# Performance work log

Measured on AMD Instinct MI355X. Metric: run time of the kernel, lower is better.

## Reference

```python
import jax, jax.numpy as jnp
import numpy as np
from jax import lax

EMB = 1024      # emb_size
H = 2 * EMB     # step_feature_width / LSTM units
B = 1024        # batch of paths
PATH_LEN = 11   # max_path_length=5 -> 5 LSTM steps
N_ENT = 100000


def setup_inputs() -> dict:
    key = jax.random.key(0)
    ks = jax.random.split(key, 8)
    s = lambda fan_in: 1.0 / np.sqrt(fan_in)
    return {
        "path": jax.random.randint(ks[0], (B, PATH_LEN), 0, N_ENT, dtype=jnp.int32),
        "emb_table": jax.random.normal(ks[1], (N_ENT, EMB), jnp.float32),
        "W_lstm": jax.random.normal(ks[2], (2 * EMB, 4 * H), jnp.float32) * s(2 * EMB),
        "U_lstm": jax.random.normal(ks[3], (H, 4 * H), jnp.float32) * s(H),
        "b_lstm": jnp.zeros((4 * H,), jnp.float32),
        "W1": jax.random.normal(ks[4], (H, 2 * EMB), jnp.float32) * s(H),
        "b1": jnp.zeros((2 * EMB,), jnp.float32),
        "W2": jax.random.normal(ks[5], (2 * EMB, 2 * EMB), jnp.float32) * s(2 * EMB),
        "b2": jnp.zeros((2 * EMB,), jnp.float32),
        "W3": jax.random.normal(ks[6], (2 * EMB, 2), jnp.float32) * s(2 * EMB),
        "b3": jnp.zeros((2,), jnp.float32),
    }


def reference(path, emb_table, W_lstm, U_lstm, b_lstm, W1, b1, W2, b2, W3, b3):
    # Gather all entity embeddings along each path: [B, PATH_LEN, EMB]
    vecs = emb_table[path]
    # Step t (t=1..5, i=2t) uses concat(vec(path[i-1]), vec(path[i])): [T, B, 2*EMB]
    x_prev = vecs[:, 1:-1:2, :]   # path[1], path[3], ...  -> [B, T, EMB]
    x_curr = vecs[:, 2::2, :]     # path[2], path[4], ...  -> [B, T, EMB]
    xs = jnp.swapaxes(jnp.concatenate([x_prev, x_curr], axis=-1), 0, 1)  # [T, B, 2E]

    def step(carry, x):
        h, c = carry
        z = x @ W_lstm + h @ U_lstm + b_lstm           # [B, 4H]
        i, f, g, o = jnp.split(z, 4, axis=-1)           # Keras gate order i,f,g,o
        i = jax.nn.sigmoid(i)
        f = jax.nn.sigmoid(f)
        g = jnp.tanh(g)
        o = jax.nn.sigmoid(o)
        c = f * c + i * g
        h = o * jnp.tanh(c)
        return (h, c), None

    h0 = jnp.zeros((xs.shape[1], H), xs.dtype)
    (h, _), _ = lax.scan(step, (h0, h0), xs)

    # 2-layer ReLU MLP + softmax head
    a = jax.nn.relu(h @ W1 + b1)
    a = jax.nn.relu(a @ W2 + b2)
    probs = jax.nn.softmax(a @ W3 + b3, axis=-1)        # [B, 2]
    return probs
```

## Files before the change

### kernel.cpp

```cpp
#include <hip/hip_runtime.h>
#include <hip/hip_bf16.h>

typedef unsigned short u16;
typedef short bf16x8 __attribute__((ext_vector_type(8)));
typedef float floatx4 __attribute__((ext_vector_type(4)));
typedef unsigned short u16x4 __attribute__((ext_vector_type(4)));
typedef unsigned short u16x8 __attribute__((ext_vector_type(8)));

__device__ __forceinline__ u16 f2bf(float f) {
    unsigned int x; __builtin_memcpy(&x, &f, 4);
    unsigned int r = x + 0x7fffu + ((x >> 16) & 1u);
    return (u16)(r >> 16);
}
__device__ __forceinline__ float sigm(float x) {
    return 1.f / (1.f + __expf(-x));
}
__device__ __forceinline__ float tanhx(float x) {
    x = fminf(fmaxf(x, -15.f), 15.f);
    float e = __expf(2.f * x);
    return (e - 1.f) / (e + 1.f);
}

__device__ __forceinline__ int permc(int c) {
    int gate = c >> 11, j = c & 2047;
    return ((j >> 4) << 6) | (gate << 4) | (j & 15);
}

__device__ __forceinline__ void async16(const void* g, void* l) {
    __builtin_amdgcn_global_load_lds(
        (__attribute__((address_space(1))) void*)(void*)(g),
        (__attribute__((address_space(3))) void*)(l),
        16, 0, 0);
}

template <bool PERM>
__global__ __launch_bounds__(256) void transpose_f32_bf16(
    const float* __restrict__ in, u16* __restrict__ out, int K, int N)
{
    __shared__ float tile[64][65];
    const int n0 = blockIdx.x * 64, k0 = blockIdx.y * 64;
    const int t = threadIdx.x;
    const int tc = t & 15, tr = t >> 4;
#pragma unroll
    for (int i = 0; i < 4; i++) {
        int k = i * 16 + tr;
        int n = tc * 4;
        float4 v = *(const float4*)&in[(size_t)(k0 + k) * N + n0 + n];
        tile[k][n + 0] = v.x; tile[k][n + 1] = v.y;
        tile[k][n + 2] = v.z; tile[k][n + 3] = v.w;
    }
    __syncthreads();
#pragma unroll
    for (int i = 0; i < 4; i++) {
        int n = i * 16 + tr;
        int k = tc * 4;
        u16x4 v;
        v.x = f2bf(tile[k + 0][n]);
        v.y = f2bf(tile[k + 1][n]);
        v.z = f2bf(tile[k + 2][n]);
        v.w = f2bf(tile[k + 3][n]);
        const int row = PERM ? permc(n0 + n) : (n0 + n);
        *(u16x4*)&out[(size_t)row * K + k0 + k] = v;
    }
}

__global__ __launch_bounds__(256) void gather_x(
    const int* __restrict__ path, const float* __restrict__ emb, u16* __restrict__ X)
{
    const int blk = blockIdx.x;
    const int t = blk >> 10, b = blk & 1023;
    const int tt = threadIdx.x;
    const int half = tt >> 7;
    const int idx = path[b * 11 + 1 + 2 * t + half];
    const int j = (tt & 127) * 8;
    const float4 v0 = *(const float4*)&emb[(size_t)idx * 1024 + j];
    const float4 v1 = *(const float4*)&emb[(size_t)idx * 1024 + j + 4];
    u16x8 o;
    o[0] = f2bf(v0.x); o[1] = f2bf(v0.y); o[2] = f2bf(v0.z); o[3] = f2bf(v0.w);
    o[4] = f2bf(v1.x); o[5] = f2bf(v1.y); o[6] = f2bf(v1.z); o[7] = f2bf(v1.w);
    *(u16x8*)&X[(size_t)blk * 2048 + half * 1024 + j] = o;
}

__global__ __launch_bounds__(256, 2) void gemm_zx(
    const u16* __restrict__ A, const u16* __restrict__ Bt,
    const float* __restrict__ bias, float* __restrict__ Cf, int M, int N, int K)
{
    __shared__ alignas(16) u16 sA[128 * 32];
    __shared__ alignas(16) u16 sB[128 * 32];
    const int t = threadIdx.x;
    const int lane = t & 63;
    const int w = t >> 6;
    const int wr = w >> 1, wc = w & 1;
    const int l15 = lane & 15, quad = lane >> 4;
    const int m0 = blockIdx.x * 128, n0 = blockIdx.y * 128;
    const int ch1 = t, ch2 = t + 256;
    const int r1 = ch1 >> 2, c1 = (ch1 & 3) * 8;
    const int r2 = ch2 >> 2, c2 = (ch2 & 3) * 8;

    floatx4 acc[4][4] = {};
    for (int k0 = 0; k0 < K; k0 += 32) {
        async16(A + (size_t)(m0 + r1) * K + k0 + c1, sA + ch1 * 8);
        async16(A + (size_t)(m0 + r2) * K + k0 + c2, sA + ch2 * 8);
        async16(Bt + (size_t)(n0 + r1) * K + k0 + c1, sB + ch1 * 8);
        async16(Bt + (size_t)(n0 + r2) * K + k0 + c2, sB + ch2 * 8);
        __syncthreads();
        bf16x8 af[4], bfr[4];
#pragma unroll
        for (int mi = 0; mi < 4; mi++)
            af[mi] = *(const bf16x8*)&sA[(wr * 64 + mi * 16 + l15) * 32 + quad * 8];
#pragma unroll
        for (int ni = 0; ni < 4; ni++)
            bfr[ni] = *(const bf16x8*)&sB[(wc * 64 + ni * 16 + l15) * 32 + quad * 8];
#pragma unroll
        for (int mi = 0; mi < 4; mi++)
#pragma unroll
            for (int ni = 0; ni < 4; ni++)
                acc[mi][ni] = __builtin_amdgcn_mfma_f32_16x16x32_bf16(
                    af[mi], bfr[ni], acc[mi][ni], 0, 0, 0);
        __syncthreads();
    }
#pragma unroll
    for (int mi = 0; mi < 4; mi++) {
#pragma unroll
        for (int ni = 0; ni < 4; ni++) {
            const int n = n0 + wc * 64 + ni * 16 + l15;
            const float bv = bias[(((n >> 4) & 3) << 11) | ((n >> 6) << 4) | (n & 15)];
#pragma unroll
            for (int r = 0; r < 4; r++) {
                const int m = m0 + wr * 64 + mi * 16 + quad * 4 + r;
                Cf[(size_t)m * N + n] = acc[mi][ni][r] + bv;
            }
        }
    }
}

__global__ __launch_bounds__(256, 2) void gemm_step(
    const u16* __restrict__ hin, const u16* __restrict__ Bt,
    const float* __restrict__ Zx, float* __restrict__ c, u16* __restrict__ hout)
{
    const int M = 1024, N = 8192, K = 2048;
    __shared__ alignas(16) u16 sA[128 * 32];
    __shared__ alignas(16) u16 sB[128 * 32];
    const int t = threadIdx.x;
    const int lane = t & 63;
    const int w = t >> 6;
    const int wr = w >> 1, wc = w & 1;
    const int l15 = lane & 15, quad = lane >> 4;
    const int m0 = blockIdx.x * 128, n0 = blockIdx.y * 128;
    const int ch1 = t, ch2 = t + 256;
    const int r1 = ch1 >> 2, c1 = (ch1 & 3) * 8;
    const int r2 = ch2 >> 2, c2 = (ch2 & 3) * 8;

    floatx4 acc[4][4] = {};
    for (int k0 = 0; k0 < K; k0 += 32) {
        async16(hin + (size_t)(m0 + r1) * K + k0 + c1, sA + ch1 * 8);
        async16(hin + (size_t)(m0 + r2) * K + k0 + c2, sA + ch2 * 8);
        async16(Bt + (size_t)(n0 + r1) * K + k0 + c1, sB + ch1 * 8);
        async16(Bt + (size_t)(n0 + r2) * K + k0 + c2, sB + ch2 * 8);
        __syncthreads();
        bf16x8 af[4], bfr[4];
#pragma unroll
        for (int mi = 0; mi < 4; mi++)
            af[mi] = *(const bf16x8*)&sA[(wr * 64 + mi * 16 + l15) * 32 + quad * 8];
#pragma unroll
        for (int ni = 0; ni < 4; ni++)
            bfr[ni] = *(const bf16x8*)&sB[(wc * 64 + ni * 16 + l15) * 32 + quad * 8];
#pragma unroll
        for (int mi = 0; mi < 4; mi++)
#pragma unroll
            for (int ni = 0; ni < 4; ni++)
                acc[mi][ni] = __builtin_amdgcn_mfma_f32_16x16x32_bf16(
                    af[mi], bfr[ni], acc[mi][ni], 0, 0, 0);
        __syncthreads();
    }

    const int jg = (n0 >> 6) + wc;
    const int j = jg * 16 + l15;
#pragma unroll
    for (int mi = 0; mi < 4; mi++) {
#pragma unroll
        for (int r = 0; r < 4; r++) {
            const int m = m0 + wr * 64 + mi * 16 + quad * 4 + r;
            const size_t zb = (size_t)m * N + jg * 64 + l15;
            const float zi = acc[mi][0][r] + Zx[zb];
            const float zf = acc[mi][1][r] + Zx[zb + 16];
            const float zg = acc[mi][2][r] + Zx[zb + 32];
            const float zo = acc[mi][3][r] + Zx[zb + 48];
            const float i_ = sigm(zi);
            const float f_ = sigm(zf);
            const float g_ = tanhx(zg);
            const float o_ = sigm(zo);
            const size_t cb = (size_t)m * 2048 + j;
            const float cn = f_ * c[cb] + i_ * g_;
            c[cb] = cn;
            hout[cb] = f2bf(o_ * tanhx(cn));
        }
    }
}

__global__ __launch_bounds__(256) void gate0(
    const float* __restrict__ Zx, float* __restrict__ c, u16* __restrict__ h)
{
    const int idx = blockIdx.x * 256 + threadIdx.x;
    const int b = idx >> 9;
    const int j = (idx & 511) * 4;
    const size_t base = (size_t)b * 8192 + ((j >> 4) << 6) + (j & 15);
    const float4 vi = *(const float4*)&Zx[base];
    const float4 vf = *(const float4*)&Zx[base + 16];
    const float4 vg = *(const float4*)&Zx[base + 32];
    const float4 vo = *(const float4*)&Zx[base + 48];
    float ia[4] = {vi.x, vi.y, vi.z, vi.w};
    float fa[4] = {vf.x, vf.y, vf.z, vf.w};
    float ga[4] = {vg.x, vg.y, vg.z, vg.w};
    float oa[4] = {vo.x, vo.y, vo.z, vo.w};
    float cn[4]; u16x4 hv;
#pragma unroll
    for (int q = 0; q < 4; q++) {
        (void)fa;
        const float i_ = sigm(ia[q]);
        const float g_ = tanhx(ga[q]);
        const float o_ = sigm(oa[q]);
        cn[q] = i_ * g_;
        hv[q] = f2bf(o_ * tanhx(cn[q]));
        (void)sigm(fa[q]);
    }
    const size_t cb = (size_t)b * 2048 + j;
    *(float4*)&c[cb] = make_float4(cn[0], cn[1], cn[2], cn[3]);
    *(u16x4*)&h[cb] = hv;
}

__global__ __launch_bounds__(256, 4) void gemm_mlp(
    const u16* __restrict__ A, const u16* __restrict__ Bt,
    const float* __restrict__ bias, u16* __restrict__ Cb, int K)
{
    const int N = 2048;
    __shared__ alignas(16) u16 sA[64 * 32];
    __shared__ alignas(16) u16 sB[128 * 32];
    const int t = threadIdx.x;
    const int lane = t & 63;
    const int w = t >> 6;
    const int wr = w >> 1, wc = w & 1;
    const int l15 = lane & 15, quad = lane >> 4;
    const int m0 = blockIdx.x * 64, n0 = blockIdx.y * 128;
    const int rA = t >> 2, cA = (t & 3) * 8;
    const int r1 = t >> 2, c1 = (t & 3) * 8;
    const int r2 = (t + 256) >> 2, c2 = ((t + 256) & 3) * 8;

    floatx4 acc[2][4] = {};
    for (int k0 = 0; k0 < K; k0 += 32) {
        async16(A + (size_t)(m0 + rA) * K + k0 + cA, sA + t * 8);
        async16(Bt + (size_t)(n0 + r1) * K + k0 + c1, sB + t * 8);
        async16(Bt + (size_t)(n0 + r2) * K + k0 + c2, sB + (t + 256) * 8);
        __syncthreads();
        bf16x8 af[2], bfr[4];
#pragma unroll
        for (int mi = 0; mi < 2; mi++)
            af[mi] = *(const bf16x8*)&sA[(wr * 32 + mi * 16 + l15) * 32 + quad * 8];
#pragma unroll
        for (int ni = 0; ni < 4; ni++)
            bfr[ni] = *(const bf16x8*)&sB[(wc * 64 + ni * 16 + l15) * 32 + quad * 8];
#pragma unroll
        for (int mi = 0; mi < 2; mi++)
#pragma unroll
            for (int ni = 0; ni < 4; ni++)
                acc[mi][ni] = __builtin_amdgcn_mfma_f32_16x16x32_bf16(
                    af[mi], bfr[ni], acc[mi][ni], 0, 0, 0);
        __syncthreads();
    }
#pragma unroll
    for (int mi = 0; mi < 2; mi++) {
#pragma unroll
        for (int ni = 0; ni < 4; ni++) {
            const int n = n0 + wc * 64 + ni * 16 + l15;
            const float bv = bias[n];
#pragma unroll
            for (int r = 0; r < 4; r++) {
                const int m = m0 + wr * 32 + mi * 16 + quad * 4 + r;
                float x = acc[mi][ni][r] + bv;
                x = x > 0.f ? x : 0.f;
                Cb[(size_t)m * N + n] = f2bf(x);
            }
        }
    }
}

__global__ __launch_bounds__(256) void head_kernel(
    const u16* __restrict__ a2, const float* __restrict__ W3,
    const float* __restrict__ b3, float* __restrict__ out)
{
    const int t = threadIdx.x;
    const int w = t >> 6, lane = t & 63;
    const int b = blockIdx.x * 4 + w;
    float s0 = 0.f, s1 = 0.f;
    for (int k = lane; k < 2048; k += 64) {
        unsigned int u = ((unsigned int)a2[(size_t)b * 2048 + k]) << 16;
        float a; __builtin_memcpy(&a, &u, 4);
        s0 += a * W3[2 * k];
        s1 += a * W3[2 * k + 1];
    }
#pragma unroll
    for (int off = 32; off > 0; off >>= 1) {
        s0 += __shfl_down(s0, off);
        s1 += __shfl_down(s1, off);
    }
    if (lane == 0) {
        const float l0 = s0 + b3[0];
        const float l1 = s1 + b3[1];
        const float m = fmaxf(l0, l1);
        const float e0 = __expf(l0 - m), e1 = __expf(l1 - m);
        const float inv = 1.f / (e0 + e1);
        out[2 * b]     = e0 * inv;
        out[2 * b + 1] = e1 * inv;
    }
}

extern "C" void kernel_launch(void* const* d_in, const int* in_sizes, int n_in,
                              void* d_out, int out_size, void* d_ws, size_t ws_size,
                              hipStream_t stream) {
    const int*   path = (const int*)d_in[0];
    const float* emb  = (const float*)d_in[1];
    const float* W    = (const float*)d_in[2];
    const float* U    = (const float*)d_in[3];
    const float* bl   = (const float*)d_in[4];
    const float* W1   = (const float*)d_in[5];
    const float* b1   = (const float*)d_in[6];
    const float* W2   = (const float*)d_in[7];
    const float* b2   = (const float*)d_in[8];
    const float* W3   = (const float*)d_in[9];
    const float* b3   = (const float*)d_in[10];

    const size_t NEED = 297795584;
    if (ws_size < NEED) return;
    char* ws = (char*)d_ws;
    u16*   Wt  = (u16*)  (ws + 0);
    u16*   Ut  = (u16*)  (ws + 33554432);
    u16*   W1t = (u16*)  (ws + 67108864);
    u16*   W2t = (u16*)  (ws + 75497472);
    u16*   X   = (u16*)  (ws + 83886080);
    float* Zx  = (float*)(ws + 104857600);
    float* c   = (float*)(ws + 272629760);
    u16*   hA  = (u16*)  (ws + 281018368);
    u16*   hB  = (u16*)  (ws + 285212672);
    u16*   a1  = (u16*)  (ws + 289406976);
    u16*   a2  = (u16*)  (ws + 293601280);

    transpose_f32_bf16<true ><<<dim3(128, 32), 256, 0, stream>>>(W, Wt, 2048, 8192);
    transpose_f32_bf16<true ><<<dim3(128, 32), 256, 0, stream>>>(U, Ut, 2048, 8192);
    transpose_f32_bf16<false><<<dim3(32, 32), 256, 0, stream>>>(W1, W1t, 2048, 2048);
    transpose_f32_bf16<false><<<dim3(32, 32), 256, 0, stream>>>(W2, W2t, 2048, 2048);
    gather_x<<<5120, 256, 0, stream>>>(path, emb, X);

    gemm_zx<<<dim3(40, 64), 256, 0, stream>>>(X, Wt, bl, Zx, 5120, 8192, 2048);

    gate0<<<2048, 256, 0, stream>>>(Zx, c, hA);
    for (int t = 1; t < 5; t++) {
        const u16* hin = (t & 1) ? hA : hB;
        u16* hout      = (t & 1) ? hB : hA;
        gemm_step<<<dim3(8, 64), 256, 0, stream>>>(
            hin, Ut, Zx + (size_t)t * 1024 * 8192, c, hout);
    }
    gemm_mlp<<<dim3(16, 16), 256, 0, stream>>>(hA, W1t, b1, a1, 2048);
    gemm_mlp<<<dim3(16, 16), 256, 0, stream>>>(a1, W2t, b2, a2, 2048);
    head_kernel<<<256, 256, 0, stream>>>(a2, W3, b3, (float*)d_out);
}
```

Measured before the change: 1.130 ms.

## Fuse first LSTM gate step into input GEMM, retile step GEMM, merge transposes

The input-projection GEMM now applies the t=0 LSTM gate math directly in its epilogue for the first 1024 rows, so it writes c and h0 without storing that slice of Zx and the separate gate0 kernel is dropped. Both GEMMs use a 1D grid with 4x4 grouped block swizzling to improve L2 reuse. The recurrent step GEMM moves to 64x128 tiles with higher occupancy, going from 512 to 1024 blocks to fill more CUs. The weight transposes are merged pairwise into two launches via blockIdx.z. Costs: a divergent epilogue and smaller per-block reuse in the step GEMM.

Measured after the change: 1.114 ms. About the same (-1.4%).

```diff
diff --git a/kernel.cpp b/kernel.cpp
--- a/kernel.cpp
+++ b/kernel.cpp
@@ -34,9 +34,12 @@
 }
 
 template <bool PERM>
-__global__ __launch_bounds__(256) void transpose_f32_bf16(
-    const float* __restrict__ in, u16* __restrict__ out, int K, int N)
-{
+__global__ __launch_bounds__(256) void transpose2(
+    const float* __restrict__ in0, const float* __restrict__ in1,
+    u16* __restrict__ out0, u16* __restrict__ out1, int K, int N)
+{
+    const float* in = blockIdx.z ? in1 : in0;
+    u16* out        = blockIdx.z ? out1 : out0;
     __shared__ float tile[64][65];
     const int n0 = blockIdx.x * 64, k0 = blockIdx.y * 64;
     const int t = threadIdx.x;
@@ -83,8 +86,10 @@
 
 __global__ __launch_bounds__(256, 2) void gemm_zx(
     const u16* __restrict__ A, const u16* __restrict__ Bt,
-    const float* __restrict__ bias, float* __restrict__ Cf, int M, int N, int K)
-{
+    const float* __restrict__ bias, float* __restrict__ Zx,
+    float* __restrict__ c, u16* __restrict__ h0)
+{
+    const int N = 8192, K = 2048;
     __shared__ alignas(16) u16 sA[128 * 32];
     __shared__ alignas(16) u16 sB[128 * 32];
     const int t = threadIdx.x;
@@ -92,7 +97,11 @@
     const int w = t >> 6;
     const int wr = w >> 1, wc = w & 1;
     const int l15 = lane & 15, quad = lane >> 4;
-    const int m0 = blockIdx.x * 128, n0 = blockIdx.y * 128;
+    const int bid = blockIdx.x;
+    const int g = bid >> 4, i = bid & 15;
+    const int mb = (g % 10) * 4 + (i & 3);
+    const int nb = (g / 10) * 4 + (i >> 2);
+    const int m0 = mb * 128, n0 = nb * 128;
     const int ch1 = t, ch2 = t + 256;
     const int r1 = ch1 >> 2, c1 = (ch1 & 3) * 8;
     const int r2 = ch2 >> 2, c2 = (ch2 & 3) * 8;
@@ -119,54 +128,80 @@
                     af[mi], bfr[ni], acc[mi][ni], 0, 0, 0);
         __syncthreads();
     }
-#pragma unroll
-    for (int mi = 0; mi < 4; mi++) {
-#pragma unroll
-        for (int ni = 0; ni < 4; ni++) {
-            const int n = n0 + wc * 64 + ni * 16 + l15;
-            const float bv = bias[(((n >> 4) & 3) << 11) | ((n >> 6) << 4) | (n & 15)];
+
+    if (m0 < 1024) {
+        const int jg = (n0 >> 6) + wc;
+        const int j = jg * 16 + l15;
+        const float bi = bias[j];
+        const float bg = bias[4096 + j];
+        const float bo = bias[6144 + j];
+#pragma unroll
+        for (int mi = 0; mi < 4; mi++) {
 #pragma unroll
             for (int r = 0; r < 4; r++) {
                 const int m = m0 + wr * 64 + mi * 16 + quad * 4 + r;
-                Cf[(size_t)m * N + n] = acc[mi][ni][r] + bv;
+                const float i_ = sigm(acc[mi][0][r] + bi);
+                const float g_ = tanhx(acc[mi][2][r] + bg);
+                const float o_ = sigm(acc[mi][3][r] + bo);
+                const float cn = i_ * g_;
+                const size_t cb = (size_t)m * 2048 + j;
+                c[cb] = cn;
+                h0[cb] = f2bf(o_ * tanhx(cn));
             }
         }
-    }
-}
-
-__global__ __launch_bounds__(256, 2) void gemm_step(
+    } else {
+#pragma unroll
+        for (int mi = 0; mi < 4; mi++) {
+#pragma unroll
+            for (int ni = 0; ni < 4; ni++) {
+                const int n = n0 + wc * 64 + ni * 16 + l15;
+                const float bv = bias[(((n >> 4) & 3) << 11) | ((n >> 6) << 4) | (n & 15)];
+#pragma unroll
+                for (int r = 0; r < 4; r++) {
+                    const int m = m0 + wr * 64 + mi * 16 + quad * 4 + r;
+                    Zx[(size_t)m * N + n] = acc[mi][ni][r] + bv;
+                }
+            }
+        }
+    }
+}
+
+__global__ __launch_bounds__(256, 4) void gemm_step(
     const u16* __restrict__ hin, const u16* __restrict__ Bt,
     const float* __restrict__ Zx, float* __restrict__ c, u16* __restrict__ hout)
 {
-    const int M = 1024, N = 8192, K = 2048;
-    __shared__ alignas(16) u16 sA[128 * 32];
+    const int N = 8192, K = 2048;
+    __shared__ alignas(16) u16 sA[64 * 32];
     __shared__ alignas(16) u16 sB[128 * 32];
     const int t = threadIdx.x;
     const int lane = t & 63;
     const int w = t >> 6;
     const int wr = w >> 1, wc = w & 1;
     const int l15 = lane & 15, quad = lane >> 4;
-    const int m0 = blockIdx.x * 128, n0 = blockIdx.y * 128;
-    const int ch1 = t, ch2 = t + 256;
-    const int r1 = ch1 >> 2, c1 = (ch1 & 3) * 8;
-    const int r2 = ch2 >> 2, c2 = (ch2 & 3) * 8;
-
-    floatx4 acc[4][4] = {};
+    const int bid = blockIdx.x;
+    const int g = bid >> 4, i = bid & 15;
+    const int mb = (g & 3) * 4 + (i & 3);
+    const int nb = (g >> 2) * 4 + (i >> 2);
+    const int m0 = mb * 64, n0 = nb * 128;
+    const int rA = t >> 2, cA = (t & 3) * 8;
+    const int r1 = t >> 2, c1 = (t & 3) * 8;
+    const int r2 = (t + 256) >> 2, c2 = ((t + 256) & 3) * 8;
+
+    floatx4 acc[2][4] = {};
     for (int k0 = 0; k0 < K; k0 += 32) {
-        async16(hin + (size_t)(m0 + r1) * K + k0 + c1, sA + ch1 * 8);
-        async16(hin + (size_t)(m0 + r2) * K + k0 + c2, sA + ch2 * 8);
-        async16(Bt + (size_t)(n0 + r1) * K + k0 + c1, sB + ch1 * 8);
-        async16(Bt + (size_t)(n0 + r2) * K + k0 + c2, sB + ch2 * 8);
-        __syncthreads();
-        bf16x8 af[4], bfr[4];
-#pragma unroll
-        for (int mi = 0; mi < 4; mi++)
-            af[mi] = *(const bf16x8*)&sA[(wr * 64 + mi * 16 + l15) * 32 + quad * 8];
+        async16(hin + (size_t)(m0 + rA) * K + k0 + cA, sA + t * 8);
+        async16(Bt + (size_t)(n0 + r1) * K + k0 + c1, sB + t * 8);
+        async16(Bt + (size_t)(n0 + r2) * K + k0 + c2, sB + (t + 256) * 8);
+        __syncthreads();
+        bf16x8 af[2], bfr[4];
+#pragma unroll
+        for (int mi = 0; mi < 2; mi++)
+            af[mi] = *(const bf16x8*)&sA[(wr * 32 + mi * 16 + l15) * 32 + quad * 8];
 #pragma unroll
         for (int ni = 0; ni < 4; ni++)
             bfr[ni] = *(const bf16x8*)&sB[(wc * 64 + ni * 16 + l15) * 32 + quad * 8];
 #pragma unroll
-        for (int mi = 0; mi < 4; mi++)
+        for (int mi = 0; mi < 2; mi++)
 #pragma unroll
             for (int ni = 0; ni < 4; ni++)
                 acc[mi][ni] = __builtin_amdgcn_mfma_f32_16x16x32_bf16(
@@ -177,10 +212,10 @@
     const int jg = (n0 >> 6) + wc;
     const int j = jg * 16 + l15;
 #pragma unroll
-    for (int mi = 0; mi < 4; mi++) {
+    for (int mi = 0; mi < 2; mi++) {
 #pragma unroll
         for (int r = 0; r < 4; r++) {
-            const int m = m0 + wr * 64 + mi * 16 + quad * 4 + r;
+            const int m = m0 + wr * 32 + mi * 16 + quad * 4 + r;
             const size_t zb = (size_t)m * N + jg * 64 + l15;
             const float zi = acc[mi][0][r] + Zx[zb];
             const float zf = acc[mi][1][r] + Zx[zb + 16];
@@ -198,37 +233,6 @@
     }
 }
 
-__global__ __launch_bounds__(256) void gate0(
-    const float* __restrict__ Zx, float* __restrict__ c, u16* __restrict__ h)
-{
-    const int idx = blockIdx.x * 256 + threadIdx.x;
-    const int b = idx >> 9;
-    const int j = (idx & 511) * 4;
-    const size_t base = (size_t)b * 8192 + ((j >> 4) << 6) + (j & 15);
-    const float4 vi = *(const float4*)&Zx[base];
-    const float4 vf = *(const float4*)&Zx[base + 16];
-    const float4 vg = *(const float4*)&Zx[base + 32];
-    const float4 vo = *(const float4*)&Zx[base + 48];
-    float ia[4] = {vi.x, vi.y, vi.z, vi.w};
-    float fa[4] = {vf.x, vf.y, vf.z, vf.w};
-    float ga[4] = {vg.x, vg.y, vg.z, vg.w};
-    float oa[4] = {vo.x, vo.y, vo.z, vo.w};
-    float cn[4]; u16x4 hv;
-#pragma unroll
-    for (int q = 0; q < 4; q++) {
-        (void)fa;
-        const float i_ = sigm(ia[q]);
-        const float g_ = tanhx(ga[q]);
-        const float o_ = sigm(oa[q]);
-        cn[q] = i_ * g_;
-        hv[q] = f2bf(o_ * tanhx(cn[q]));
-        (void)sigm(fa[q]);
-    }
-    const size_t cb = (size_t)b * 2048 + j;
-    *(float4*)&c[cb] = make_float4(cn[0], cn[1], cn[2], cn[3]);
-    *(u16x4*)&h[cb] = hv;
-}
-
 __global__ __launch_bounds__(256, 4) void gemm_mlp(
     const u16* __restrict__ A, const u16* __restrict__ Bt,
     const float* __restrict__ bias, u16* __restrict__ Cb, int K)
@@ -344,19 +348,16 @@
     u16*   a1  = (u16*)  (ws + 289406976);
     u16*   a2  = (u16*)  (ws + 293601280);
 
-    transpose_f32_bf16<true ><<<dim3(128, 32), 256, 0, stream>>>(W, Wt, 2048, 8192);
-    transpose_f32_bf16<true ><<<dim3(128, 32), 256, 0, stream>>>(U, Ut, 2048, 8192);
-    transpose_f32_bf16<false><<<dim3(32, 32), 256, 0, stream>>>(W1, W1t, 2048, 2048);
-    transpose_f32_bf16<false><<<dim3(32, 32), 256, 0, stream>>>(W2, W2t, 2048, 2048);
+    transpose2<true ><<<dim3(128, 32, 2), 256, 0, stream>>>(W, U, Wt, Ut, 2048, 8192);
+    transpose2<false><<<dim3(32, 32, 2), 256, 0, stream>>>(W1, W2, W1t, W2t, 2048, 2048);
     gather_x<<<5120, 256, 0, stream>>>(path, emb, X);
 
-    gemm_zx<<<dim3(40, 64), 256, 0, stream>>>(X, Wt, bl, Zx, 5120, 8192, 2048);
-
-    gate0<<<2048, 256, 0, stream>>>(Zx, c, hA);
+    gemm_zx<<<2560, 256, 0, stream>>>(X, Wt, bl, Zx, c, hA);
+
     for (int t = 1; t < 5; t++) {
         const u16* hin = (t & 1) ? hA : hB;
         u16* hout      = (t & 1) ? hB : hA;
-        gemm_step<<<dim3(8, 64), 256, 0, stream>>>(
+        gemm_step<<<1024, 256, 0, stream>>>(
             hin, Ut, Zx + (size_t)t * 1024 * 8192, c, hout);
     }
     gemm_mlp<<<dim3(16, 16), 256, 0, stream>>>(hA, W1t, b1, a1, 2048);
```
